# Optimization experiments

Measured on AMD Instinct MI355X. Metric: run time of the kernel, lower is better.

The kernel has to match this reference:

```python
import jax, jax.numpy as jnp
import numpy as np

NB_KNN = (10, 20, 100, 200)   # values of k to evaluate; max_k = 200
T = 0.07                       # softmax temperature
NUM_CLASSES = 1000


def setup_inputs() -> dict:
    key = jax.random.key(0)
    k1, k2, k3 = jax.random.split(key, 3)
    features_rank = jax.random.normal(k1, (256, 512), jnp.float32)      # (B, d) query features
    train_features = jax.random.normal(k2, (100000, 512), jnp.float32)  # (N, d) train bank
    train_labels = jax.random.randint(k3, (100000,), 0, NUM_CLASSES)     # (N,) int labels
    return {"features_rank": features_rank, "train_features": train_features,
            "train_labels": train_labels}


def _knn_probs(features_rank, train_features, train_labels):
    max_k = max(NB_KNN)
    # similarity: (B, N) = (B, d) @ (d, N)  -- mirrors torch.mm(broadcasted, train_features_rank_T)
    sims = features_rank @ train_features.T
    topk_sims, idx = jax.lax.top_k(sims, max_k)          # (B, max_k), sorted descending
    neighbors = train_labels[idx]                         # (B, max_k) gathered labels
    w = jax.nn.softmax(topk_sims / T, axis=1)             # (B, max_k) neighbor weights
    B = features_rank.shape[0]
    rows = jnp.arange(B)[:, None]                         # (B, 1) row indices for scatter
    # Instead of materializing one_hot (B, max_k, C) and summing prefixes,
    # scatter-add the first k weights into per-class buckets (same math, fused).
    probs = [jnp.zeros((B, NUM_CLASSES), w.dtype).at[rows, neighbors[:, :k]].add(w[:, :k])
             for k in NB_KNN]
    return jnp.stack(probs, axis=0)                       # (len(NB_KNN), B, C)


def reference(features_rank, train_features, train_labels):
    return _knn_probs(features_rank, train_features, train_labels)
```

## Files before the change

### kernel.cpp

```cpp
#include <hip/hip_runtime.h>
#include <math.h>

#define KDIM   512
#define NCLS   1000
#define CUTOFF 3.0f
#define MAXCAP 4096
#define BN     64
#define NCHUNK (KDIM / 32)

typedef __attribute__((ext_vector_type(8))) short  short8;
typedef __attribute__((ext_vector_type(4))) float  floatx4;

__device__ __forceinline__ unsigned enc_f(float f) {
    unsigned u = __float_as_uint(f);
    return (u & 0x80000000u) ? ~u : (u | 0x80000000u);
}
__device__ __forceinline__ float dec_f(unsigned k) {
    unsigned u = (k & 0x80000000u) ? (k & 0x7FFFFFFFu) : ~k;
    return __uint_as_float(u);
}
__device__ __forceinline__ unsigned short f2bf(float f) {
    unsigned u = __float_as_uint(f);
    u += 0x7FFFu + ((u >> 16) & 1u);
    return (unsigned short)(u >> 16);
}
__device__ __forceinline__ float bf2f(unsigned short h) {
    return __uint_as_float(((unsigned)h) << 16);
}

__global__ void k_prep(const float* __restrict__ A, unsigned short* __restrict__ af,
                       unsigned* __restrict__ cnt, unsigned* __restrict__ gmax, int Brows) {
    int t = blockIdx.x * blockDim.x + threadIdx.x;
    if (t < Brows) { cnt[t] = 0u; gmax[t] = enc_f(-3.0e38f); }
    if (t >= Brows * (KDIM / 8)) return;
    int r = t >> 6;
    int o = t & 63;
    int s16 = r >> 4, c = o >> 2, kq = o & 3;
    int lane = kq * 16 + (r & 15);
    const float* src = A + (size_t)r * KDIM + o * 8;
    size_t bhi = ((size_t)((s16 * 16 + c) * 2 + 0) * 64 + lane) * 8;
    size_t blo = ((size_t)((s16 * 16 + c) * 2 + 1) * 64 + lane) * 8;
#pragma unroll
    for (int j = 0; j < 8; ++j) {
        float f = src[j];
        unsigned short h = f2bf(f);
        af[bhi + j] = h;
        af[blo + j] = f2bf(f - bf2f(h));
    }
}

__global__ __launch_bounds__(256, 2) void k_gemm(
    const float* __restrict__ Bt,
    const unsigned short* __restrict__ af,
    float* __restrict__ cand_val, int* __restrict__ cand_idx,
    unsigned* __restrict__ cnt, unsigned* __restrict__ gmax,
    int N, int cap)
{
    const int tid  = threadIdx.x;
    const int lane = tid & 63;
    const int wid  = tid >> 6;
    const int colBase = blockIdx.x * BN;
    const int q    = lane >> 4;
    const int n15  = lane & 15;

    const float* bp[4];
#pragma unroll
    for (int ct = 0; ct < 4; ++ct) {
        int c = colBase + ct * 16 + n15;
        if (c > N - 1) c = N - 1;
        bp[ct] = Bt + (size_t)c * KDIM + q * 8;
    }
    const unsigned short* ap[4];
#pragma unroll
    for (int rt = 0; rt < 4; ++rt)
        ap[rt] = af + (size_t)(wid * 4 + rt) * 16384 + lane * 8;

    floatx4 acc[4][4];
#pragma unroll
    for (int rt = 0; rt < 4; ++rt)
#pragma unroll
        for (int ct = 0; ct < 4; ++ct)
            acc[rt][ct] = (floatx4){0.f, 0.f, 0.f, 0.f};

    float4 Bf[2][4][2];
#pragma unroll
    for (int ct = 0; ct < 4; ++ct) {
        Bf[0][ct][0] = *(const float4*)(bp[ct]);
        Bf[0][ct][1] = *(const float4*)(bp[ct] + 4);
    }

#pragma unroll 2
    for (int cg = 0; cg < NCHUNK; ++cg) {
        const int cur = cg & 1, nxt = cur ^ 1;

        short8 aH[4], aL[4];
#pragma unroll
        for (int rt = 0; rt < 4; ++rt) {
            const unsigned short* p = ap[rt] + cg * 1024;
            aH[rt] = *(const short8*)(p);
            aL[rt] = *(const short8*)(p + 512);
        }
        if (cg < NCHUNK - 1) {
#pragma unroll
            for (int ct = 0; ct < 4; ++ct) {
                const float* p = bp[ct] + (cg + 1) * 32;
                Bf[nxt][ct][0] = *(const float4*)(p);
                Bf[nxt][ct][1] = *(const float4*)(p + 4);
            }
        }
        short8 bh[4], bl[4];
#pragma unroll
        for (int ct = 0; ct < 4; ++ct) {
            union { float4 v[2]; float f[8]; } P;
            union { short8 v; unsigned short u[8]; } H, L;
            P.v[0] = Bf[cur][ct][0]; P.v[1] = Bf[cur][ct][1];
#pragma unroll
            for (int j = 0; j < 8; ++j) {
                unsigned short h = f2bf(P.f[j]);
                H.u[j] = h; L.u[j] = f2bf(P.f[j] - bf2f(h));
            }
            bh[ct] = H.v; bl[ct] = L.v;
        }
#pragma unroll
        for (int ct = 0; ct < 4; ++ct)
#pragma unroll
            for (int rt = 0; rt < 4; ++rt) {
                acc[rt][ct] = __builtin_amdgcn_mfma_f32_16x16x32_bf16(aH[rt], bh[ct], acc[rt][ct], 0, 0, 0);
                acc[rt][ct] = __builtin_amdgcn_mfma_f32_16x16x32_bf16(aH[rt], bl[ct], acc[rt][ct], 0, 0, 0);
                acc[rt][ct] = __builtin_amdgcn_mfma_f32_16x16x32_bf16(aL[rt], bh[ct], acc[rt][ct], 0, 0, 0);
            }
    }

#pragma unroll
    for (int rt = 0; rt < 4; ++rt) {
#pragma unroll
        for (int reg = 0; reg < 4; ++reg) {
            const int row = (wid * 4 + rt) * 16 + q * 4 + reg;
            float m = fmaxf(fmaxf(acc[rt][0][reg], acc[rt][1][reg]),
                            fmaxf(acc[rt][2][reg], acc[rt][3][reg]));
#pragma unroll
            for (int off = 1; off < 16; off <<= 1) m = fmaxf(m, __shfl_xor(m, off));
            unsigned oldk = 0u;
            if (n15 == 0) oldk = atomicMax(&gmax[row], enc_f(m));
            oldk = (unsigned)__shfl((int)oldk, lane & 48);
            const float thr = fmaxf(dec_f(oldk), m) - CUTOFF;
#pragma unroll
            for (int ct = 0; ct < 4; ++ct) {
                const float v = acc[rt][ct][reg];
                const int col = colBase + ct * 16 + n15;
                if (v >= thr && col < N) {
                    unsigned p = atomicAdd(&cnt[row], 1u);
                    if (p < (unsigned)cap) {
                        cand_val[(size_t)row * cap + p] = v;
                        cand_idx[(size_t)row * cap + p] = col;
                    }
                }
            }
        }
    }
}

__global__ __launch_bounds__(256) void k_finalize(
    const float* __restrict__ cand_val,
    const int* __restrict__ cand_idx,
    const unsigned* __restrict__ cnt,
    const unsigned* __restrict__ gmax,
    const int* __restrict__ labels,
    float* __restrict__ out,
    int Brows, int cap)
{
    __shared__ float s_val[256];
    __shared__ int   s_idx[256];
    __shared__ int   s_n;
    const int row = blockIdx.x;
    const int tid = threadIdx.x;
    if (tid == 0) s_n = 0;
    __syncthreads();

    const float m   = dec_f(gmax[row]);
    const float thr = m - CUTOFF;
    const int n = min((int)cnt[row], cap);
    for (int i = tid; i < n; i += 256) {
        float v = cand_val[(size_t)row * cap + i];
        if (v >= thr) {
            int p = atomicAdd(&s_n, 1);
            if (p < 256) { s_val[p] = v; s_idx[p] = cand_idx[(size_t)row * cap + i]; }
        }
    }
    __syncthreads();

    for (int c = tid; c < 4 * NCLS; c += 256) {
        int s = c / NCLS, cc = c - s * NCLS;
        out[(size_t)s * ((size_t)Brows * NCLS) + (size_t)row * NCLS + cc] = 0.f;
    }
    __syncthreads();

    if (tid == 0) {
        int ns = min(s_n, 256);
        for (int i = 1; i < ns; ++i) {
            float v = s_val[i]; int ix = s_idx[i];
            int j = i - 1;
            while (j >= 0 && s_val[j] < v) { s_val[j+1] = s_val[j]; s_idx[j+1] = s_idx[j]; --j; }
            s_val[j+1] = v; s_idx[j+1] = ix;
        }
        if (ns > 200) ns = 200;
        float Z = 0.f;
        for (int i = 0; i < ns; ++i) Z += expf((s_val[i] - m) / 0.07f);
        float invZ = 1.f / Z;
        const int kv[4] = {10, 20, 100, 200};
        for (int i = 0; i < ns; ++i) {
            float w = expf((s_val[i] - m) / 0.07f) * invZ;
            int lab = labels[s_idx[i]];
#pragma unroll
            for (int s = 0; s < 4; ++s)
                if (i < kv[s])
                    out[(size_t)s * ((size_t)Brows * NCLS) + (size_t)row * NCLS + lab] += w;
        }
    }
}

extern "C" void kernel_launch(void* const* d_in, const int* in_sizes, int n_in,
                              void* d_out, int out_size, void* d_ws, size_t ws_size,
                              hipStream_t stream) {
    const float* A      = (const float*)d_in[0];
    const float* Bt     = (const float*)d_in[1];
    const int*   labels = (const int*)d_in[2];
    float* out = (float*)d_out;

    const int Brows = in_sizes[0] / KDIM;
    const int N     = in_sizes[2];

    size_t af_elems = (size_t)Brows * KDIM * 2;
    unsigned short* af = (unsigned short*)d_ws;
    unsigned* cnt  = (unsigned*)(af + af_elems);
    unsigned* gmax = cnt + Brows;
    char* rest = (char*)(gmax + Brows);
    size_t used  = (size_t)(rest - (char*)d_ws);
    size_t avail = (ws_size > used) ? (ws_size - used) : 0;
    int cap = (int)((avail / ((size_t)Brows * 8)) < (size_t)MAXCAP
                        ? (avail / ((size_t)Brows * 8)) : (size_t)MAXCAP);
    if (cap < 1) cap = 1;
    float* cand_val = (float*)rest;
    int*   cand_idx = (int*)(cand_val + (size_t)Brows * cap);

    k_prep<<<(Brows * (KDIM / 8) + 255) / 256, 256, 0, stream>>>(A, af, cnt, gmax, Brows);
    k_gemm<<<(N + BN - 1) / BN, 256, 0, stream>>>(Bt, af, cand_val, cand_idx, cnt, gmax, N, cap);
    k_finalize<<<Brows, 256, 0, stream>>>(cand_val, cand_idx, cnt, gmax, labels, out, Brows, cap);
}
```

Before: 465.2 us.

## Screen candidates with single bf16 GEMM and rescore survivors in fp32

Replaces the three-pass split-bf16 GEMM with one bf16 pass and a wider cutoff margin, so the similarity matrix is only used to screen candidates. Surviving candidates are rescored exactly in fp32 in the finalize kernel before sorting and softmax. B tiles are now staged through LDS with direct global-to-LDS loads in a swizzled layout, and B is truncated to bf16 rather than rounded. Occupancy is raised to 3 blocks per CU. The goal is to cut MFMA and conversion work by about two thirds. The risk is that the bf16 screening error exceeds the margin, or that more candidates overflow the 256-entry buffer.

```diff
diff --git a/kernel.cpp b/kernel.cpp
--- a/kernel.cpp
+++ b/kernel.cpp
@@ -3,10 +3,10 @@
 
 #define KDIM   512
 #define NCLS   1000
-#define CUTOFF 3.0f
+#define CUTOFF 3.7f
 #define MAXCAP 4096
 #define BN     64
-#define NCHUNK (KDIM / 32)
+#define NST    16
 
 typedef __attribute__((ext_vector_type(8))) short  short8;
 typedef __attribute__((ext_vector_type(4))) float  floatx4;
@@ -24,8 +24,11 @@
     u += 0x7FFFu + ((u >> 16) & 1u);
     return (unsigned short)(u >> 16);
 }
-__device__ __forceinline__ float bf2f(unsigned short h) {
-    return __uint_as_float(((unsigned)h) << 16);
+
+__device__ __forceinline__ void glds16(const float* g, unsigned* l) {
+    __builtin_amdgcn_global_load_lds(
+        (const __attribute__((address_space(1))) unsigned*)g,
+        (__attribute__((address_space(3))) unsigned*)l, 16, 0, 0);
 }
 
 __global__ void k_prep(const float* __restrict__ A, unsigned short* __restrict__ af,
@@ -35,45 +38,37 @@
     if (t >= Brows * (KDIM / 8)) return;
     int r = t >> 6;
     int o = t & 63;
-    int s16 = r >> 4, c = o >> 2, kq = o & 3;
+    int s16 = r >> 4, cg = o >> 2, kq = o & 3;
     int lane = kq * 16 + (r & 15);
     const float* src = A + (size_t)r * KDIM + o * 8;
-    size_t bhi = ((size_t)((s16 * 16 + c) * 2 + 0) * 64 + lane) * 8;
-    size_t blo = ((size_t)((s16 * 16 + c) * 2 + 1) * 64 + lane) * 8;
-#pragma unroll
-    for (int j = 0; j < 8; ++j) {
-        float f = src[j];
-        unsigned short h = f2bf(f);
-        af[bhi + j] = h;
-        af[blo + j] = f2bf(f - bf2f(h));
-    }
-}
-
-__global__ __launch_bounds__(256, 2) void k_gemm(
+    size_t b = ((size_t)(s16 * 16 + cg) * 64 + lane) * 8;
+#pragma unroll
+    for (int j = 0; j < 8; ++j) af[b + j] = f2bf(src[j]);
+}
+
+__global__ __launch_bounds__(256, 3) void k_gemm(
     const float* __restrict__ Bt,
     const unsigned short* __restrict__ af,
     float* __restrict__ cand_val, int* __restrict__ cand_idx,
     unsigned* __restrict__ cnt, unsigned* __restrict__ gmax,
     int N, int cap)
 {
+    __shared__ unsigned Bs[2][2048];
+
     const int tid  = threadIdx.x;
     const int lane = tid & 63;
-    const int wid  = tid >> 6;
-    const int colBase = blockIdx.x * BN;
+    const int w    = tid >> 6;
     const int q    = lane >> 4;
     const int n15  = lane & 15;
-
-    const float* bp[4];
-#pragma unroll
-    for (int ct = 0; ct < 4; ++ct) {
-        int c = colBase + ct * 16 + n15;
-        if (c > N - 1) c = N - 1;
-        bp[ct] = Bt + (size_t)c * KDIM + q * 8;
-    }
-    const unsigned short* ap[4];
-#pragma unroll
-    for (int rt = 0; rt < 4; ++rt)
-        ap[rt] = af + (size_t)(wid * 4 + rt) * 16384 + lane * 8;
+    const int colBase = blockIdx.x * BN;
+
+    const int s0 = tid, s1 = tid + 256;
+    const int c0 = s0 >> 3, c1 = s1 >> 3;
+    const int q40 = (s0 & 7) ^ (c0 & 7), q41 = (s1 & 7) ^ (c1 & 7);
+    int gc0 = colBase + c0; if (gc0 > N - 1) gc0 = N - 1;
+    int gc1 = colBase + c1; if (gc1 > N - 1) gc1 = N - 1;
+    const float* g0 = Bt + (size_t)gc0 * KDIM + q40 * 4;
+    const float* g1 = Bt + (size_t)gc1 * KDIM + q41 * 4;
 
     floatx4 acc[4][4];
 #pragma unroll
@@ -82,60 +77,51 @@
         for (int ct = 0; ct < 4; ++ct)
             acc[rt][ct] = (floatx4){0.f, 0.f, 0.f, 0.f};
 
-    float4 Bf[2][4][2];
-#pragma unroll
-    for (int ct = 0; ct < 4; ++ct) {
-        Bf[0][ct][0] = *(const float4*)(bp[ct]);
-        Bf[0][ct][1] = *(const float4*)(bp[ct] + 4);
-    }
+    glds16(g0, &Bs[0][s0 * 4]);
+    glds16(g1, &Bs[0][s1 * 4]);
 
 #pragma unroll 2
-    for (int cg = 0; cg < NCHUNK; ++cg) {
-        const int cur = cg & 1, nxt = cur ^ 1;
-
-        short8 aH[4], aL[4];
-#pragma unroll
-        for (int rt = 0; rt < 4; ++rt) {
-            const unsigned short* p = ap[rt] + cg * 1024;
-            aH[rt] = *(const short8*)(p);
-            aL[rt] = *(const short8*)(p + 512);
-        }
-        if (cg < NCHUNK - 1) {
-#pragma unroll
-            for (int ct = 0; ct < 4; ++ct) {
-                const float* p = bp[ct] + (cg + 1) * 32;
-                Bf[nxt][ct][0] = *(const float4*)(p);
-                Bf[nxt][ct][1] = *(const float4*)(p + 4);
-            }
-        }
-        short8 bh[4], bl[4];
+    for (int ks = 0; ks < NST; ++ks) {
+        __syncthreads();
+
+        short8 aH[4];
+#pragma unroll
+        for (int rt = 0; rt < 4; ++rt)
+            aH[rt] = *(const short8*)(af + ((size_t)((w * 4 + rt) * 16 + ks) * 64 + lane) * 8);
+
+        if (ks + 1 < NST) {
+            glds16(g0 + (ks + 1) * 32, &Bs[(ks + 1) & 1][s0 * 4]);
+            glds16(g1 + (ks + 1) * 32, &Bs[(ks + 1) & 1][s1 * 4]);
+        }
+
+        const unsigned* bs = Bs[ks & 1];
+        short8 bh[4];
 #pragma unroll
         for (int ct = 0; ct < 4; ++ct) {
-            union { float4 v[2]; float f[8]; } P;
-            union { short8 v; unsigned short u[8]; } H, L;
-            P.v[0] = Bf[cur][ct][0]; P.v[1] = Bf[cur][ct][1];
-#pragma unroll
-            for (int j = 0; j < 8; ++j) {
-                unsigned short h = f2bf(P.f[j]);
-                H.u[j] = h; L.u[j] = f2bf(P.f[j] - bf2f(h));
-            }
-            bh[ct] = H.v; bl[ct] = L.v;
+            const int col = ct * 16 + n15;
+            const int g2 = col & 7, base = col * 8;
+            union { float4 f; unsigned u[4]; } A0, A1;
+            A0.f = *(const float4*)&bs[(base + ((2 * q) ^ g2)) * 4];
+            A1.f = *(const float4*)&bs[(base + ((2 * q + 1) ^ g2)) * 4];
+            union { unsigned u[4]; short8 v; } R;
+            R.u[0] = (A0.u[1] & 0xFFFF0000u) | (A0.u[0] >> 16);
+            R.u[1] = (A0.u[3] & 0xFFFF0000u) | (A0.u[2] >> 16);
+            R.u[2] = (A1.u[1] & 0xFFFF0000u) | (A1.u[0] >> 16);
+            R.u[3] = (A1.u[3] & 0xFFFF0000u) | (A1.u[2] >> 16);
+            bh[ct] = R.v;
         }
 #pragma unroll
         for (int ct = 0; ct < 4; ++ct)
 #pragma unroll
-            for (int rt = 0; rt < 4; ++rt) {
+            for (int rt = 0; rt < 4; ++rt)
                 acc[rt][ct] = __builtin_amdgcn_mfma_f32_16x16x32_bf16(aH[rt], bh[ct], acc[rt][ct], 0, 0, 0);
-                acc[rt][ct] = __builtin_amdgcn_mfma_f32_16x16x32_bf16(aH[rt], bl[ct], acc[rt][ct], 0, 0, 0);
-                acc[rt][ct] = __builtin_amdgcn_mfma_f32_16x16x32_bf16(aL[rt], bh[ct], acc[rt][ct], 0, 0, 0);
-            }
     }
 
 #pragma unroll
     for (int rt = 0; rt < 4; ++rt) {
 #pragma unroll
         for (int reg = 0; reg < 4; ++reg) {
-            const int row = (wid * 4 + rt) * 16 + q * 4 + reg;
+            const int row = (w * 4 + rt) * 16 + q * 4 + reg;
             float m = fmaxf(fmaxf(acc[rt][0][reg], acc[rt][1][reg]),
                             fmaxf(acc[rt][2][reg], acc[rt][3][reg]));
 #pragma unroll
@@ -161,6 +147,8 @@
 }
 
 __global__ __launch_bounds__(256) void k_finalize(
+    const float* __restrict__ A,
+    const float* __restrict__ Bt,
     const float* __restrict__ cand_val,
     const int* __restrict__ cand_idx,
     const unsigned* __restrict__ cnt,
@@ -171,14 +159,16 @@
 {
     __shared__ float s_val[256];
     __shared__ int   s_idx[256];
+    __shared__ float s_arow[KDIM];
     __shared__ int   s_n;
     const int row = blockIdx.x;
     const int tid = threadIdx.x;
     if (tid == 0) s_n = 0;
+    for (int i = tid; i < KDIM; i += 256) s_arow[i] = A[(size_t)row * KDIM + i];
     __syncthreads();
 
-    const float m   = dec_f(gmax[row]);
-    const float thr = m - CUTOFF;
+    const float ma  = dec_f(gmax[row]);
+    const float thr = ma - CUTOFF;
     const int n = min((int)cnt[row], cap);
     for (int i = tid; i < n; i += 256) {
         float v = cand_val[(size_t)row * cap + i];
@@ -189,6 +179,18 @@
     }
     __syncthreads();
 
+    const int ns = min(s_n, 256);
+    const int wv = tid >> 6, l = tid & 63;
+    for (int i = wv; i < ns; i += 4) {
+        const float* brow = Bt + (size_t)s_idx[i] * KDIM;
+        float p = 0.f;
+#pragma unroll
+        for (int j = 0; j < 8; ++j) p += s_arow[l * 8 + j] * brow[l * 8 + j];
+#pragma unroll
+        for (int off = 1; off < 64; off <<= 1) p += __shfl_xor(p, off);
+        if (l == 0) s_val[i] = p;
+    }
+
     for (int c = tid; c < 4 * NCLS; c += 256) {
         int s = c / NCLS, cc = c - s * NCLS;
         out[(size_t)s * ((size_t)Brows * NCLS) + (size_t)row * NCLS + cc] = 0.f;
@@ -196,25 +198,26 @@
     __syncthreads();
 
     if (tid == 0) {
-        int ns = min(s_n, 256);
-        for (int i = 1; i < ns; ++i) {
+        int m = ns;
+        for (int i = 1; i < m; ++i) {
             float v = s_val[i]; int ix = s_idx[i];
             int j = i - 1;
             while (j >= 0 && s_val[j] < v) { s_val[j+1] = s_val[j]; s_idx[j+1] = s_idx[j]; --j; }
             s_val[j+1] = v; s_idx[j+1] = ix;
         }
-        if (ns > 200) ns = 200;
+        if (m > 200) m = 200;
+        const float mx = s_val[0];
         float Z = 0.f;
-        for (int i = 0; i < ns; ++i) Z += expf((s_val[i] - m) / 0.07f);
+        for (int i = 0; i < m; ++i) Z += expf((s_val[i] - mx) / 0.07f);
         float invZ = 1.f / Z;
         const int kv[4] = {10, 20, 100, 200};
-        for (int i = 0; i < ns; ++i) {
-            float w = expf((s_val[i] - m) / 0.07f) * invZ;
+        for (int i = 0; i < m; ++i) {
+            float wgt = expf((s_val[i] - mx) / 0.07f) * invZ;
             int lab = labels[s_idx[i]];
 #pragma unroll
             for (int s = 0; s < 4; ++s)
                 if (i < kv[s])
-                    out[(size_t)s * ((size_t)Brows * NCLS) + (size_t)row * NCLS + lab] += w;
+                    out[(size_t)s * ((size_t)Brows * NCLS) + (size_t)row * NCLS + lab] += wgt;
         }
     }
 }
@@ -230,20 +233,20 @@
     const int Brows = in_sizes[0] / KDIM;
     const int N     = in_sizes[2];
 
-    size_t af_elems = (size_t)Brows * KDIM * 2;
+    size_t af_elems = (size_t)Brows * KDIM;
     unsigned short* af = (unsigned short*)d_ws;
     unsigned* cnt  = (unsigned*)(af + af_elems);
     unsigned* gmax = cnt + Brows;
     char* rest = (char*)(gmax + Brows);
     size_t used  = (size_t)(rest - (char*)d_ws);
     size_t avail = (ws_size > used) ? (ws_size - used) : 0;
-    int cap = (int)((avail / ((size_t)Brows * 8)) < (size_t)MAXCAP
-                        ? (avail / ((size_t)Brows * 8)) : (size_t)MAXCAP);
+    size_t pairs = avail / ((size_t)Brows * 8);
+    int cap = (int)(pairs < (size_t)MAXCAP ? pairs : (size_t)MAXCAP);
     if (cap < 1) cap = 1;
     float* cand_val = (float*)rest;
     int*   cand_idx = (int*)(cand_val + (size_t)Brows * cap);
 
     k_prep<<<(Brows * (KDIM / 8) + 255) / 256, 256, 0, stream>>>(A, af, cnt, gmax, Brows);
     k_gemm<<<(N + BN - 1) / BN, 256, 0, stream>>>(Bt, af, cand_val, cand_idx, cnt, gmax, N, cap);
-    k_finalize<<<Brows, 256, 0, stream>>>(cand_val, cand_idx, cnt, gmax, labels, out, Brows, cap);
-}
+    k_finalize<<<Brows, 256, 0, stream>>>(A, Bt, cand_val, cand_idx, cnt, gmax, labels, out, Brows, cap);
+}
```

After: 457.8 us. About the same (-1.6%).
